# Kernel tuning notes

Hardware: AMD Instinct MI355X
Metric: run time of the kernel (lower is better)

## Reference

```python
import jax, jax.numpy as jnp
import numpy as np

EPS = 1e-5

def _layernorm(x, g, b):
    mu = jnp.mean(x, axis=-1, keepdims=True)
    var = jnp.var(x, axis=-1, keepdims=True)
    return (x - mu) * jax.lax.rsqrt(var + EPS) * g + b

def _attn(x, Wq, bq, Wk, bk, Wv, bv):
    # torch Linear: y = x @ W.T + b, W is [out, in]
    q = jnp.einsum('bse,oe->bso', x, Wq) + bq
    k = jnp.einsum('bse,oe->bso', x, Wk) + bk
    v = jnp.einsum('bse,oe->bso', x, Wv) + bv
    S = x.shape[1]
    # NOTE: original scales by sqrt(seq_len) (the 'C' dim), reproduced faithfully
    att = jnp.einsum('bqd,bkd->bqk', q, k) / jnp.sqrt(jnp.asarray(S, x.dtype))
    att = jax.nn.softmax(att, axis=-1)
    return jnp.einsum('bqk,bkd->bqd', att, v)

def setup_inputs() -> dict:
    key = jax.random.key(0)
    ks = jax.random.split(key, 16)
    B, S, E = 4, 4096, 256
    sc = 1.0 / np.sqrt(E)
    d = {'x': jax.random.normal(ks[0], (B, S, E), jnp.float32)}
    names = ['Wq1', 'Wk1', 'Wv1', 'Wq2', 'Wk2', 'Wv2']
    for i, n in enumerate(names):
        d[n] = jax.random.normal(ks[1 + i], (E, E), jnp.float32) * sc
        d['b' + n[1:]] = jnp.zeros((E,), jnp.float32)
    d['g1'] = jnp.ones((E,), jnp.float32)
    d['beta1'] = jnp.zeros((E,), jnp.float32)
    d['g2'] = jnp.ones((E,), jnp.float32)
    d['beta2'] = jnp.zeros((E,), jnp.float32)
    return d

def reference(x, Wq1, bq1, Wk1, bk1, Wv1, bv1, Wq2, bq2, Wk2, bk2, Wv2, bv2, g1, beta1, g2, beta2):
    o = _layernorm(_attn(x, Wq1, bq1, Wk1, bk1, Wv1, bv1) + x, g1, beta1)
    f = _attn(o, Wq2, bq2, Wk2, bk2, Wv2, bv2)
    return _layernorm(f + o, g2, beta2)
```

## Files before the change

kernel.cpp:

```cpp
#include <hip/hip_runtime.h>
#include <hip/hip_bf16.h>


typedef __attribute__((ext_vector_type(8))) short bf16x8;
typedef __attribute__((ext_vector_type(4))) float f32x4;
typedef __attribute__((ext_vector_type(16))) float f32x16;
typedef __attribute__((ext_vector_type(4))) int i32x4;
typedef __attribute__((ext_vector_type(8))) int i32x8;
typedef unsigned char u8;

#define MFMA_BF16(A, B, C) __builtin_amdgcn_mfma_f32_16x16x32_bf16(A, B, C, 0, 0, 0)
#define MFMA_SC(A, B, C, SA, SB)                                                \
    __builtin_amdgcn_mfma_scale_f32_32x32x64_f8f6f4(A, B, C, 0, 0, 0, SA, 0, SB)
#define SCALE_1  0x7F7F7F7Fu
#define SCALE_Q  0x79797979u

#define CP16(g, l)                                                              \
    __builtin_amdgcn_global_load_lds(                                           \
        (const __attribute__((address_space(1))) void*)(g),                     \
        (__attribute__((address_space(3))) void*)(l), 16, 0, 0)

static __device__ __forceinline__ short f2bf(float f) {
    __hip_bfloat16 h = __float2bfloat16(f);
    return __builtin_bit_cast(short, h);
}
static __device__ __forceinline__ float bf2f(short s) {
    unsigned int u = ((unsigned int)(unsigned short)s) << 16;
    return __builtin_bit_cast(float, u);
}
static __device__ __forceinline__ float ld1(const float* p) { return *p; }
static __device__ __forceinline__ float ld1(const short* p) { return bf2f(*p); }
static __device__ __forceinline__ void st1(float* p, float v) { *p = v; }
static __device__ __forceinline__ void st1(short* p, float v) { *p = f2bf(v); }

static __device__ __forceinline__ u8 f2fp8(float f) {
    return (u8)(__builtin_amdgcn_cvt_pk_fp8_f32(f, f, 0, false) & 0xff);
}
static __device__ __forceinline__ unsigned int pk4fp8(float a, float b, float c, float d) {
    int w = __builtin_amdgcn_cvt_pk_fp8_f32(a, b, 0, false);
    w = __builtin_amdgcn_cvt_pk_fp8_f32(c, d, w, true);
    return (unsigned int)w;
}

static __device__ __forceinline__ bf16x8 ldA8(const short* p) {
    return *reinterpret_cast<const bf16x8*>(p);
}
static __device__ __forceinline__ bf16x8 ldA8(const float* p) {
    float4 f0 = *reinterpret_cast<const float4*>(p);
    float4 f1 = *reinterpret_cast<const float4*>(p + 4);
    bf16x8 r;
    r[0] = f2bf(f0.x); r[1] = f2bf(f0.y); r[2] = f2bf(f0.z); r[3] = f2bf(f0.w);
    r[4] = f2bf(f1.x); r[5] = f2bf(f1.y); r[6] = f2bf(f1.z); r[7] = f2bf(f1.w);
    return r;
}

static __device__ __forceinline__ i32x8 cat(i32x4 lo, i32x4 hi) {
    i32x8 r;
    r[0] = lo[0]; r[1] = lo[1]; r[2] = lo[2]; r[3] = lo[3];
    r[4] = hi[0]; r[5] = hi[1]; r[6] = hi[2]; r[7] = hi[3];
    return r;
}

template <int NCH256>
static __device__ __forceinline__ void stage_rows(const short* __restrict__ g,
                                                  short* s, int tid) {
    const int wave = tid >> 6;
#pragma unroll
    for (int j = 0; j < NCH256; ++j) {
        const int idx = j * 256 + tid;
        const int row = idx >> 5, c = idx & 31;
        CP16(g + row * 256 + ((c ^ (row & 7)) << 3),
             s + ((j * 256 + wave * 64) << 3));
    }
}
static __device__ __forceinline__ void stage_k(const u8* __restrict__ g,
                                               u8* s, int tid) {
    const int wave = tid >> 6;
#pragma unroll
    for (int j = 0; j < 4; ++j) {
        const int idx = j * 256 + tid;
        CP16(g + (idx << 4), s + ((j * 256 + wave * 64) << 4));
    }
}
static __device__ __forceinline__ void stage_v(const u8* __restrict__ g,
                                               u8* s, int tid) {
    const int wave = tid >> 6;
#pragma unroll
    for (int j = 0; j < 4; ++j) {
        const int idx = j * 256 + tid;
        CP16(g + ((idx >> 2) * 4096) + ((idx & 3) << 4),
             s + ((j * 256 + wave * 64) << 4));
    }
}

__global__ __launch_bounds__(256) void cvt_w_kernel(
    const float* __restrict__ w0, const float* __restrict__ w1,
    const float* __restrict__ w2, const float* __restrict__ w3,
    const float* __restrict__ w4, const float* __restrict__ w5,
    short* __restrict__ wb)
{
    const int idx = (blockIdx.x * 256 + threadIdx.x) * 8;
    const int w = idx >> 16, off = idx & 65535;
    const float* src = w0;
    if (w == 1) src = w1;
    else if (w == 2) src = w2;
    else if (w == 3) src = w3;
    else if (w == 4) src = w4;
    else if (w == 5) src = w5;
    *reinterpret_cast<bf16x8*>(wb + w * 65536 + off) = ldA8(src + off);
}

template <typename TX>
__global__ __launch_bounds__(256, 2) void qkv_proj_kernel(
    const TX* __restrict__ X, const short* __restrict__ Wb,
    const float* __restrict__ bq, const float* __restrict__ bk,
    const float* __restrict__ bv,
    u8* __restrict__ Qo, u8* __restrict__ Ko, u8* __restrict__ VTo)
{
    __shared__ __attribute__((aligned(16))) short Wt[128 * 256];
    const int tid  = threadIdx.x;
    const int lane = tid & 63;
    const int wave = tid >> 6;
    const int c16  = lane & 15;
    const int quad = lane >> 4;
    const int which = blockIdx.y;
    const int m0 = blockIdx.x * 64 + wave * 16;

    const short* W    = Wb + which * 65536;
    const float* bias = (which == 0) ? bq : (which == 1) ? bk : bv;

    bf16x8 a[8];
#pragma unroll
    for (int ke = 0; ke < 8; ++ke)
        a[ke] = ldA8(X + (m0 + c16) * 256 + ke * 32 + quad * 8);

    f32x4 acc[16];
#pragma unroll
    for (int nb = 0; nb < 16; ++nb) { f32x4 z = {0.f, 0.f, 0.f, 0.f}; acc[nb] = z; }

#pragma unroll
    for (int half = 0; half < 2; ++half) {
        if (half) __syncthreads();
        stage_rows<16>(W + half * 128 * 256, Wt, tid);
        __syncthreads();
#pragma unroll
        for (int nb8 = 0; nb8 < 8; ++nb8) {
            const int nb = half * 8 + nb8;
            const short* wr = Wt + (nb8 * 16 + c16) * 256;
#pragma unroll
            for (int ke = 0; ke < 8; ++ke) {
                bf16x8 b = *reinterpret_cast<const bf16x8*>(
                    wr + (((ke * 4 + quad) ^ (c16 & 7)) << 3));
                acc[nb] = MFMA_BF16(a[ke], b, acc[nb]);
            }
        }
    }

    if (which == 0) {
        constexpr float L2E = 1.4426950408889634f;
#pragma unroll
        for (int nb = 0; nb < 16; ++nb) {
            const int o = nb * 16 + c16;
            const float bb_ = bias[o];
#pragma unroll
            for (int r = 0; r < 4; ++r)
                Qo[(m0 + quad * 4 + r) * 256 + o] = f2fp8((acc[nb][r] + bb_) * L2E);
        }
    } else if (which == 1) {
#pragma unroll
        for (int nb = 0; nb < 16; ++nb) {
            const int o = nb * 16 + c16;
            const float bb_ = bias[o];
#pragma unroll
            for (int r = 0; r < 4; ++r) {
                const int row = m0 + quad * 4 + r;
                Ko[row * 256 + (((nb ^ (row & 15)) << 4) | c16)] =
                    f2fp8(acc[nb][r] + bb_);
            }
        }
    } else {
#pragma unroll
        for (int nb = 0; nb < 16; ++nb) {
            const int o = nb * 16 + c16;
            const float bb_ = bias[o];
            const int row = m0 + quad * 4;
            const int batch = row >> 12;
            const int n = row & 4095;
            const int nsw = (n & ~63) | ((((n >> 4) ^ (o >> 1)) & 3) << 4) |
                            (n & 12);
            unsigned int pk = pk4fp8(acc[nb][0] + bb_, acc[nb][1] + bb_,
                                     acc[nb][2] + bb_, acc[nb][3] + bb_);
            *reinterpret_cast<unsigned int*>(
                VTo + (size_t)batch * (256 * 4096) + o * 4096 + nsw) = pk;
        }
    }
}

__global__ __launch_bounds__(256, 2) void attn_part_kernel(
    const u8* __restrict__ Qb, const u8* __restrict__ Kb,
    const u8* __restrict__ VTb,
    short* __restrict__ Op, float* __restrict__ Lo)
{
    __shared__ __attribute__((aligned(16))) u8 Kt[2][64 * 256];
    __shared__ __attribute__((aligned(16))) u8 Vt[2][256 * 64];

    const int tid  = threadIdx.x;
    const int lane = tid & 63;
    const int wave = tid >> 6;
    const int l31  = lane & 31;
    const int hi   = lane >> 5;
    const int c16  = lane & 15;
    const int bi = blockIdx.x;
    const int combo = ((bi & 7) << 1) | (bi >> 8);
    const int batch = combo >> 2;
    const int ks    = combo & 3;
    const int qt    = (bi >> 3) & 31;
    const size_t bb = (size_t)batch * (4096 * 256);
    const int rw = qt * 128 + wave * 32;
    const int kbase = ks * 1024;

    i32x8 qf[4];
#pragma unroll
    for (int ke = 0; ke < 4; ++ke) {
        const u8* qp = Qb + bb + (rw + l31) * 256 + ke * 64 + hi * 32;
        qf[ke] = cat(*reinterpret_cast<const i32x4*>(qp),
                     *reinterpret_cast<const i32x4*>(qp + 16));
    }

    f32x16 z16;
#pragma unroll
    for (int i = 0; i < 16; ++i) z16[i] = 0.f;
    f32x16 oa[8];
#pragma unroll
    for (int et = 0; et < 8; ++et) oa[et] = z16;
    f32x16 lacc = z16;

    i32x8 onesf;
#pragma unroll
    for (int i = 0; i < 8; ++i) onesf[i] = 0x38383838;

    int kx0[4], kx1[4];
#pragma unroll
    for (int ke = 0; ke < 4; ++ke) {
        kx0[ke] = ((ke * 4 + hi * 2) ^ c16) << 4;
        kx1[ke] = ((ke * 4 + hi * 2 + 1) ^ c16) << 4;
    }
    const int vsw = (l31 >> 1) & 3;
    const int vx0 = ((hi * 2) ^ vsw) << 4;
    const int vx1 = ((hi * 2 + 1) ^ vsw) << 4;

    const u8* Kg = Kb + bb + kbase * 256;
    const u8* Vg = VTb + bb + kbase;

    f32x16 s0, s1;
    auto compute_st = [&](const u8* K) {
        const u8* kp = K + l31 * 256;
        s0 = z16; s1 = z16;
        __builtin_amdgcn_s_setprio(1);
#pragma unroll
        for (int ke = 0; ke < 4; ++ke) {
            i32x8 a0 = cat(*reinterpret_cast<const i32x4*>(kp + kx0[ke]),
                           *reinterpret_cast<const i32x4*>(kp + kx1[ke]));
            s0 = MFMA_SC(a0, qf[ke], s0, SCALE_1, SCALE_Q);
            i32x8 a1 = cat(*reinterpret_cast<const i32x4*>(kp + 8192 + kx0[ke]),
                           *reinterpret_cast<const i32x4*>(kp + 8192 + kx1[ke]));
            s1 = MFMA_SC(a1, qf[ke], s1, SCALE_1, SCALE_Q);
        }
        __builtin_amdgcn_s_setprio(0);
    };

    stage_k(Kg, &Kt[0][0], tid);
    stage_v(Vg, &Vt[0][0], tid);
    __syncthreads();
    compute_st(&Kt[0][0]);
    stage_k(Kg + 64 * 256, &Kt[1][0], tid);
    stage_v(Vg + 64, &Vt[1][0], tid);

    for (int kt = 0; kt < 16; ++kt) {
        unsigned int dw0[4], dw1[4];
#pragma unroll
        for (int g = 0; g < 4; ++g) {
            const float p00 = exp2f(s0[4 * g + 0]);
            const float p01 = exp2f(s0[4 * g + 1]);
            const float p02 = exp2f(s0[4 * g + 2]);
            const float p03 = exp2f(s0[4 * g + 3]);
            const float p10 = exp2f(s1[4 * g + 0]);
            const float p11 = exp2f(s1[4 * g + 1]);
            const float p12 = exp2f(s1[4 * g + 2]);
            const float p13 = exp2f(s1[4 * g + 3]);
            dw0[g] = pk4fp8(p00, p01, p02, p03);
            dw1[g] = pk4fp8(p10, p11, p12, p13);
        }
#pragma unroll
        for (int g = 0; g < 4; ++g)
            asm volatile("v_permlane32_swap_b32 %0, %1"
                         : "+v"(dw0[g]), "+v"(dw1[g]));
        i32x8 pf;
        pf[0] = (int)dw0[0]; pf[1] = (int)dw1[0];
        pf[2] = (int)dw0[1]; pf[3] = (int)dw1[1];
        pf[4] = (int)dw0[2]; pf[5] = (int)dw1[2];
        pf[6] = (int)dw0[3]; pf[7] = (int)dw1[3];

        {
            const u8* V = &Vt[kt & 1][0];
            __builtin_amdgcn_s_setprio(1);
#pragma unroll
            for (int et = 0; et < 8; ++et) {
                const u8* vp = V + (et * 32 + l31) * 64;
                i32x8 b = cat(*reinterpret_cast<const i32x4*>(vp + vx0),
                              *reinterpret_cast<const i32x4*>(vp + vx1));
                oa[et] = MFMA_SC(pf, b, oa[et], SCALE_1, SCALE_1);
            }
            lacc = MFMA_SC(pf, onesf, lacc, SCALE_1, SCALE_1);
            __builtin_amdgcn_s_setprio(0);
        }

        if (kt < 15) {
            __syncthreads();
            if (kt < 14) {
                stage_k(Kg + (kt + 2) * 64 * 256, &Kt[kt & 1][0], tid);
                stage_v(Vg + (kt + 2) * 64, &Vt[kt & 1][0], tid);
            }
            compute_st(&Kt[(kt + 1) & 1][0]);
        }
    }

    const size_t base = (size_t)ks * 16384 + batch * 4096 + rw;
#pragma unroll
    for (int et = 0; et < 8; ++et)
#pragma unroll
        for (int r = 0; r < 16; ++r) {
            const int qr = (r & 3) + 8 * (r >> 2) + 4 * hi;
            Op[(base + qr) * 256 + et * 32 + l31] = f2bf(oa[et][r]);
        }
    if (l31 == 0) {
#pragma unroll
        for (int r = 0; r < 16; ++r) {
            const int qr = (r & 3) + 8 * (r >> 2) + 4 * hi;
            Lo[base + qr] = lacc[r];
        }
    }
}

template <typename TRES, typename TOUT>
__global__ __launch_bounds__(256) void merge_ln_kernel(
    const short* __restrict__ Op, const float* __restrict__ Lo,
    const TRES* __restrict__ res, const float* __restrict__ gamma,
    const float* __restrict__ beta, TOUT* __restrict__ out)
{
    const int lane = threadIdx.x & 63;
    const int wave = threadIdx.x >> 6;
    const int row = blockIdx.x * 4 + wave;
    const float li = 1.0f / (Lo[row] + Lo[16384 + row] +
                             Lo[32768 + row] + Lo[49152 + row]);
    const int e = lane * 4;
    float o[4] = {0.f, 0.f, 0.f, 0.f};
#pragma unroll
    for (int s = 0; s < 4; ++s) {
        ushort4 u = *reinterpret_cast<const ushort4*>(
            Op + ((size_t)s * 16384 + row) * 256 + e);
        o[0] += bf2f((short)u.x);
        o[1] += bf2f((short)u.y);
        o[2] += bf2f((short)u.z);
        o[3] += bf2f((short)u.w);
    }
    float y[4];
#pragma unroll
    for (int i = 0; i < 4; ++i)
        y[i] = o[i] * li + ld1(res + (size_t)row * 256 + e + i);

    float sum = y[0] + y[1] + y[2] + y[3];
    float sq  = y[0]*y[0] + y[1]*y[1] + y[2]*y[2] + y[3]*y[3];
#pragma unroll
    for (int d = 1; d < 64; d <<= 1) {
        sum += __shfl_xor(sum, d, 64);
        sq  += __shfl_xor(sq,  d, 64);
    }
    const float mean = sum * (1.0f / 256.0f);
    const float var  = sq * (1.0f / 256.0f) - mean * mean;
    const float rstd = rsqrtf(var + 1e-5f);
#pragma unroll
    for (int i = 0; i < 4; ++i)
        st1(out + (size_t)row * 256 + e + i,
            (y[i] - mean) * rstd * gamma[e + i] + beta[e + i]);
}

extern "C" void kernel_launch(void* const* d_in, const int* in_sizes, int n_in,
                              void* d_out, int out_size, void* d_ws, size_t ws_size,
                              hipStream_t stream) {
    const float* x   = (const float*)d_in[0];
    const float* Wq1 = (const float*)d_in[1];
    const float* bq1 = (const float*)d_in[2];
    const float* Wk1 = (const float*)d_in[3];
    const float* bk1 = (const float*)d_in[4];
    const float* Wv1 = (const float*)d_in[5];
    const float* bv1 = (const float*)d_in[6];
    const float* Wq2 = (const float*)d_in[7];
    const float* bq2 = (const float*)d_in[8];
    const float* Wk2 = (const float*)d_in[9];
    const float* bk2 = (const float*)d_in[10];
    const float* Wv2 = (const float*)d_in[11];
    const float* bv2 = (const float*)d_in[12];
    const float* g1  = (const float*)d_in[13];
    const float* be1 = (const float*)d_in[14];
    const float* g2  = (const float*)d_in[15];
    const float* be2 = (const float*)d_in[16];

    const size_t NE = (size_t)16384 * 256;
    short* O1  = (short*)d_ws;
    short* Wb  = O1 + NE;
    u8*    Qb  = (u8*)(Wb + 6 * 65536);
    u8*    Kb  = Qb + NE;
    u8*    VTb = Kb + NE;
    short* Op  = (short*)(VTb + NE);
    float* Lo  = (float*)(Op + 4 * NE);
    float* outp = (float*)d_out;

    dim3 pgrid(256, 3), pblk(256);

    cvt_w_kernel<<<192, 256, 0, stream>>>(Wq1, Wk1, Wv1, Wq2, Wk2, Wv2, Wb);

    qkv_proj_kernel<float><<<pgrid, pblk, 0, stream>>>(
        x, Wb, bq1, bk1, bv1, Qb, Kb, VTb);
    attn_part_kernel<<<512, 256, 0, stream>>>(Qb, Kb, VTb, Op, Lo);
    merge_ln_kernel<float, short><<<4096, 256, 0, stream>>>(Op, Lo, x, g1, be1, O1);

    qkv_proj_kernel<short><<<pgrid, pblk, 0, stream>>>(
        O1, Wb + 3 * 65536, bq2, bk2, bv2, Qb, Kb, VTb);
    attn_part_kernel<<<512, 256, 0, stream>>>(Qb, Kb, VTb, Op, Lo);
    merge_ln_kernel<short, float><<<4096, 256, 0, stream>>>(Op, Lo, O1, g2, be2, outp);
}
```

Baseline: 238.2 us.

## Software-pipeline QK^T of next tile with PV of current tile in attention loop

The attention main loop is reordered so the QK^T MFMAs for tile kt+1 are issued right after the barrier, ahead of the PV MFMAs for tile kt. The exp2 and fp8 packing for tile kt+1 now run after PV, which gives the matrix unit independent work while the softmax of the previous tile finishes. K and V staging are split so V is prefetched one tile ahead and K two tiles ahead. The change also swaps exp2f for the raw hardware v_exp_f32 builtin, and seeds the first MFMA of each S tile directly from zero instead of clearing the accumulator first. This adds register pressure, since S for the next tile and the current P fragment are live at the same time, and it depends on the barrier ordering still covering the async LDS loads.

```diff
diff --git a/kernel.cpp b/kernel.cpp
--- a/kernel.cpp
+++ b/kernel.cpp
@@ -19,6 +19,18 @@
     __builtin_amdgcn_global_load_lds(                                           \
         (const __attribute__((address_space(1))) void*)(g),                     \
         (__attribute__((address_space(3))) void*)(l), 16, 0, 0)
+
+#if __has_builtin(__builtin_amdgcn_exp2f)
+static __device__ __forceinline__ float fexp2(float x) {
+    return __builtin_amdgcn_exp2f(x);
+}
+#else
+static __device__ __forceinline__ float fexp2(float x) {
+    float r;
+    asm("v_exp_f32 %0, %1" : "=v"(r) : "v"(x));
+    return r;
+}
+#endif
 
 static __device__ __forceinline__ short f2bf(float f) {
     __hip_bfloat16 h = __float2bfloat16(f);
@@ -253,41 +265,36 @@
     const u8* Vg = VTb + bb + kbase;
 
     f32x16 s0, s1;
-    auto compute_st = [&](const u8* K) {
+    i32x8 pf;
+
+    auto do_st = [&](const u8* K) {
         const u8* kp = K + l31 * 256;
-        s0 = z16; s1 = z16;
         __builtin_amdgcn_s_setprio(1);
 #pragma unroll
         for (int ke = 0; ke < 4; ++ke) {
             i32x8 a0 = cat(*reinterpret_cast<const i32x4*>(kp + kx0[ke]),
                            *reinterpret_cast<const i32x4*>(kp + kx1[ke]));
-            s0 = MFMA_SC(a0, qf[ke], s0, SCALE_1, SCALE_Q);
+            s0 = (ke == 0) ? MFMA_SC(a0, qf[0], z16, SCALE_1, SCALE_Q)
+                           : MFMA_SC(a0, qf[ke], s0, SCALE_1, SCALE_Q);
             i32x8 a1 = cat(*reinterpret_cast<const i32x4*>(kp + 8192 + kx0[ke]),
                            *reinterpret_cast<const i32x4*>(kp + 8192 + kx1[ke]));
-            s1 = MFMA_SC(a1, qf[ke], s1, SCALE_1, SCALE_Q);
+            s1 = (ke == 0) ? MFMA_SC(a1, qf[0], z16, SCALE_1, SCALE_Q)
+                           : MFMA_SC(a1, qf[ke], s1, SCALE_1, SCALE_Q);
         }
         __builtin_amdgcn_s_setprio(0);
     };
-
-    stage_k(Kg, &Kt[0][0], tid);
-    stage_v(Vg, &Vt[0][0], tid);
-    __syncthreads();
-    compute_st(&Kt[0][0]);
-    stage_k(Kg + 64 * 256, &Kt[1][0], tid);
-    stage_v(Vg + 64, &Vt[1][0], tid);
-
-    for (int kt = 0; kt < 16; ++kt) {
+    auto do_softmax = [&]() {
         unsigned int dw0[4], dw1[4];
 #pragma unroll
         for (int g = 0; g < 4; ++g) {
-            const float p00 = exp2f(s0[4 * g + 0]);
-            const float p01 = exp2f(s0[4 * g + 1]);
-            const float p02 = exp2f(s0[4 * g + 2]);
-            const float p03 = exp2f(s0[4 * g + 3]);
-            const float p10 = exp2f(s1[4 * g + 0]);
-            const float p11 = exp2f(s1[4 * g + 1]);
-            const float p12 = exp2f(s1[4 * g + 2]);
-            const float p13 = exp2f(s1[4 * g + 3]);
+            const float p00 = fexp2(s0[4 * g + 0]);
+            const float p01 = fexp2(s0[4 * g + 1]);
+            const float p02 = fexp2(s0[4 * g + 2]);
+            const float p03 = fexp2(s0[4 * g + 3]);
+            const float p10 = fexp2(s1[4 * g + 0]);
+            const float p11 = fexp2(s1[4 * g + 1]);
+            const float p12 = fexp2(s1[4 * g + 2]);
+            const float p13 = fexp2(s1[4 * g + 3]);
             dw0[g] = pk4fp8(p00, p01, p02, p03);
             dw1[g] = pk4fp8(p10, p11, p12, p13);
         }
@@ -295,11 +302,28 @@
         for (int g = 0; g < 4; ++g)
             asm volatile("v_permlane32_swap_b32 %0, %1"
                          : "+v"(dw0[g]), "+v"(dw1[g]));
-        i32x8 pf;
         pf[0] = (int)dw0[0]; pf[1] = (int)dw1[0];
         pf[2] = (int)dw0[1]; pf[3] = (int)dw1[1];
         pf[4] = (int)dw0[2]; pf[5] = (int)dw1[2];
         pf[6] = (int)dw0[3]; pf[7] = (int)dw1[3];
+    };
+
+    stage_k(Kg, &Kt[0][0], tid);
+    stage_v(Vg, &Vt[0][0], tid);
+    __syncthreads();
+    stage_k(Kg + 64 * 256, &Kt[1][0], tid);
+    do_st(&Kt[0][0]);
+    do_softmax();
+
+    for (int kt = 0; kt < 16; ++kt) {
+        __syncthreads();
+        if (kt + 2 < 16)
+            stage_k(Kg + (kt + 2) * 64 * 256, &Kt[kt & 1][0], tid);
+        if (kt + 1 < 16)
+            stage_v(Vg + (kt + 1) * 64, &Vt[(kt + 1) & 1][0], tid);
+
+        if (kt + 1 < 16)
+            do_st(&Kt[(kt + 1) & 1][0]);
 
         {
             const u8* V = &Vt[kt & 1][0];
@@ -315,14 +339,8 @@
             __builtin_amdgcn_s_setprio(0);
         }
 
-        if (kt < 15) {
-            __syncthreads();
-            if (kt < 14) {
-                stage_k(Kg + (kt + 2) * 64 * 256, &Kt[kt & 1][0], tid);
-                stage_v(Vg + (kt + 2) * 64, &Vt[kt & 1][0], tid);
-            }
-            compute_st(&Kt[(kt + 1) & 1][0]);
-        }
+        if (kt + 1 < 16)
+            do_softmax();
     }
 
     const size_t base = (size_t)ks * 16384 + batch * 4096 + rw;
```

Result: slower. 243.5 us (+2.2%).
